# Kernel tuning notes

Hardware: AMD Instinct MI355X
Metric: run time of the kernel (lower is better)

## Reference

```python
import jax, jax.numpy as jnp
import numpy as np

B, T, C = 4, 4096, 512
DFF = 4 * C


def setup_inputs() -> dict:
    key = jax.random.key(0)
    ks = jax.random.split(key, 8)
    s = 1.0 / np.sqrt(C)
    sf = 1.0 / np.sqrt(DFF)
    return {
        "inputs": jax.random.normal(ks[0], (B, T, C), dtype=jnp.float32),
        "Wq": jax.random.uniform(ks[1], (C, C), jnp.float32, -s, s),
        "Wk": jax.random.uniform(ks[2], (C, C), jnp.float32, -s, s),
        "Wv": jax.random.uniform(ks[3], (C, C), jnp.float32, -s, s),
        "W1": jax.random.uniform(ks[4], (C, DFF), jnp.float32, -s, s),
        "b1": jax.random.uniform(ks[5], (DFF,), jnp.float32, -s, s),
        "W2": jax.random.uniform(ks[6], (DFF, C), jnp.float32, -sf, sf),
        "b2": jax.random.uniform(ks[7], (C,), jnp.float32, -sf, sf),
    }


def reference(inputs, Wq, Wk, Wv, W1, b1, W2, b2):
    # Single-head causal self-attention, NO 1/sqrt(d) scaling (faithful to source)
    q = inputs @ Wq  # [B,T,C]
    k = inputs @ Wk
    v = inputs @ Wv
    scores = jnp.einsum("btc,bsc->bts", q, k)  # [B,T,T]
    Tdim = inputs.shape[1]
    causal = jnp.tril(jnp.ones((Tdim, Tdim), dtype=bool))
    scores = jnp.where(causal, scores, -jnp.inf)
    attn = jax.nn.softmax(scores, axis=-1)
    new_v = jnp.einsum("bts,bsc->btc", attn, v)  # [B,T,C]
    h = jax.nn.relu(new_v @ W1 + b1)  # [B,T,4C]
    return h @ W2 + b2  # [B,T,C]
```

## Files before the change

kernel.cpp:

```cpp
#include <hip/hip_runtime.h>
#include <stdint.h>

typedef __attribute__((ext_vector_type(8))) short bf16x8;
typedef __attribute__((ext_vector_type(8))) _Float16 f16x8;
typedef __attribute__((ext_vector_type(4))) float f32x4;
typedef __attribute__((ext_vector_type(4))) unsigned short us4;
typedef unsigned short u16;

#define DEVI static __device__ __forceinline__

#define Bb 4
#define Tt 4096
#define Cch 512
#define DFFd 2048
#define Mrows (Bb*Tt)
#define TRI 8650752ull

DEVI u16 f2bf(float f){
  union{float f;unsigned u;} v; v.f = f;
  unsigned r = v.u + 0x7FFFu + ((v.u >> 16) & 1u);
  return (u16)(r >> 16);
}
DEVI u16 f2h(float f){
  union{_Float16 h; u16 u;} v; v.h = (_Float16)f; return v.u;
}
DEVI float h2f(u16 h){
  union{u16 u; _Float16 h;} v; v.u = h; return (float)v.h;
}
DEVI size_t PANE(int q){ return (size_t)8192 * (size_t)(q*(q+1)); }

DEVI void gload16(const void* g, void* l){
  __builtin_amdgcn_global_load_lds((const __attribute__((address_space(1))) unsigned int*)g,
                                   (__attribute__((address_space(3))) unsigned int*)l, 16, 0, 0);
}

#define RDSWZ(l15, l4) (((l4)*16) ^ ((((l15) >> 1) & 3) << 4))
#define SRCSWZ(lane) ((((lane) & 3)*8) ^ ((((lane) >> 3) & 3) << 3))

DEVI void stage256x64_w8(const u16* __restrict__ base, int ld, char* lds, int w, int lane){
  #pragma unroll
  for(int i = 0; i < 4; i++){
    int s = i & 1;
    int chunk = w + (i >> 1)*8;
    int row = chunk*16 + (lane >> 2);
    int col = s*32 + SRCSWZ(lane);
    gload16(base + (size_t)row * ld + col, lds + s*16384 + chunk*1024 + lane*16);
  }
}
DEVI void stage128x64_w8(const u16* __restrict__ base, int ld, char* lds, int w, int lane){
  #pragma unroll
  for(int i = 0; i < 2; i++){
    int s = i;
    int row = w*16 + (lane >> 2);
    int col = s*32 + SRCSWZ(lane);
    gload16(base + (size_t)row * ld + col, lds + s*8192 + w*1024 + lane*16);
  }
}

__global__ void k_cast_f16(const float* __restrict__ in, u16* __restrict__ out, int n){
  int i = (blockIdx.x * blockDim.x + threadIdx.x) * 4;
  if(i < n){
    float4 f = *(const float4*)(in + i);
    us4 o; o.x = f2h(f.x); o.y = f2h(f.y); o.z = f2h(f.z); o.w = f2h(f.w);
    *(us4*)(out + i) = o;
  }
}

__global__ void k_transpose_f32_f16(const float* __restrict__ in, u16* __restrict__ out,
                                    int inStride, int outStride){
  __shared__ float tile[32][33];
  int c0 = blockIdx.x * 32, r0 = blockIdx.y * 32;
  int tx = threadIdx.x, ty = threadIdx.y;
  #pragma unroll
  for(int j = 0; j < 4; j++)
    tile[ty + 8*j][tx] = in[(size_t)(r0 + ty + 8*j) * inStride + c0 + tx];
  __syncthreads();
  #pragma unroll
  for(int j = 0; j < 4; j++)
    out[(size_t)(c0 + ty + 8*j) * outStride + r0 + tx] = f2h(tile[tx][ty + 8*j]);
}

__global__ void k_transpose_f32_bf16(const float* __restrict__ in, u16* __restrict__ out,
                                     int inStride, int outStride){
  __shared__ float tile[32][33];
  int c0 = blockIdx.x * 32, r0 = blockIdx.y * 32;
  int tx = threadIdx.x, ty = threadIdx.y;
  #pragma unroll
  for(int j = 0; j < 4; j++)
    tile[ty + 8*j][tx] = in[(size_t)(r0 + ty + 8*j) * inStride + c0 + tx];
  __syncthreads();
  #pragma unroll
  for(int j = 0; j < 4; j++)
    out[(size_t)(c0 + ty + 8*j) * outStride + r0 + tx] = f2bf(tile[tx][ty + 8*j]);
}

DEVI void core_f16_256(const u16* __restrict__ A, const u16* __restrict__ B,
                       int lda, int ldb, int K, u16* As, u16* Bs, f32x4 (&acc)[4][4]){
  const int t = threadIdx.x;
  const int lane = t & 63, w = t >> 6;
  const int l15 = lane & 15, l4 = lane >> 4;
  const int wr = (w >> 1) * 64, wc = (w & 1) * 64;
  const int ro = RDSWZ(l15, l4);
  for(int kt = 0; kt < K; kt += 64){
    __syncthreads();
    stage256x64_w8(A + kt, lda, (char*)As, w, lane);
    stage128x64_w8(B + kt, ldb, (char*)Bs, w, lane);
    __syncthreads();
    f16x8 af[2][4], bfr[2][4];
    #pragma unroll
    for(int s = 0; s < 2; s++){
      #pragma unroll
      for(int mi = 0; mi < 4; mi++)
        af[s][mi] = *(const f16x8*)((const char*)As + s*16384 + (wr + mi*16 + l15)*64 + ro);
      #pragma unroll
      for(int ni = 0; ni < 4; ni++)
        bfr[s][ni] = *(const f16x8*)((const char*)Bs + s*8192 + (wc + ni*16 + l15)*64 + ro);
    }
    #pragma unroll
    for(int s = 0; s < 2; s++)
      #pragma unroll
      for(int mi = 0; mi < 4; mi++)
        #pragma unroll
        for(int ni = 0; ni < 4; ni++)
          acc[mi][ni] = __builtin_amdgcn_mfma_f32_16x16x32_f16(af[s][mi], bfr[s][ni], acc[mi][ni], 0, 0, 0);
  }
}

DEVI void core_bf16_256(const u16* __restrict__ A, const u16* __restrict__ B,
                        int lda, int ldb, int K, u16* As, u16* Bs, f32x4 (&acc)[4][4]){
  const int t = threadIdx.x;
  const int lane = t & 63, w = t >> 6;
  const int l15 = lane & 15, l4 = lane >> 4;
  const int wr = (w >> 1) * 64, wc = (w & 1) * 64;
  const int ro = RDSWZ(l15, l4);
  for(int kt = 0; kt < K; kt += 64){
    __syncthreads();
    stage256x64_w8(A + kt, lda, (char*)As, w, lane);
    stage128x64_w8(B + kt, ldb, (char*)Bs, w, lane);
    __syncthreads();
    bf16x8 af[2][4], bfr[2][4];
    #pragma unroll
    for(int s = 0; s < 2; s++){
      #pragma unroll
      for(int mi = 0; mi < 4; mi++)
        af[s][mi] = *(const bf16x8*)((const char*)As + s*16384 + (wr + mi*16 + l15)*64 + ro);
      #pragma unroll
      for(int ni = 0; ni < 4; ni++)
        bfr[s][ni] = *(const bf16x8*)((const char*)Bs + s*8192 + (wc + ni*16 + l15)*64 + ro);
    }
    #pragma unroll
    for(int s = 0; s < 2; s++)
      #pragma unroll
      for(int mi = 0; mi < 4; mi++)
        #pragma unroll
        for(int ni = 0; ni < 4; ni++)
          acc[mi][ni] = __builtin_amdgcn_mfma_f32_16x16x32_bf16(af[s][mi], bfr[s][ni], acc[mi][ni], 0, 0, 0);
  }
}

__global__ __launch_bounds__(512) void k_qkv(const u16* __restrict__ Xf,
                                             const u16* __restrict__ Wt,
                                             u16* __restrict__ QK,
                                             u16* __restrict__ Vg){
  __shared__ u16 As[16384], Bs[8192];
  const int bm = blockIdx.x * 256, bn = blockIdx.y * 128;
  f32x4 acc[4][4] = {};
  core_f16_256(Xf + (size_t)bm*512, Wt + (size_t)bn*512, 512, 512, 512, As, Bs, acc);
  const int t = threadIdx.x, lane = t & 63, w = t >> 6;
  const int l15 = lane & 15, l4 = lane >> 4;
  const int wr = (w >> 1) * 64, wc = (w & 1) * 64;
  #pragma unroll
  for(int mi = 0; mi < 4; mi++)
    #pragma unroll
    for(int ni = 0; ni < 4; ni++){
      int col = bn + wc + ni*16 + l15;
      #pragma unroll
      for(int r = 0; r < 4; r++){
        int row = bm + wr + mi*16 + l4*4 + r;
        u16 h = f2h(acc[mi][ni][r]);
        if(col < 1024){
          QK[(size_t)row * 1024 + col] = h;
        } else {
          int c = col - 1024;
          int b = row >> 12, tq = row & 4095;
          Vg[(size_t)b*Cch*Tt + ((size_t)(tq >> 5) * 512 + c) * 32 + (tq & 31)] = h;
        }
      }
    }
}

__global__ __launch_bounds__(512) void k_score(const u16* __restrict__ QK, int b0,
                                               u16* __restrict__ Sp){
  const int kt = blockIdx.x, qy = 15 - blockIdx.y;
  if(kt > 2*qy + 1) return;
  const int zb = blockIdx.z;
  const u16* QKb = QK + (size_t)(b0 + zb) * Tt * 1024;
  u16* Spz = Sp + (size_t)zb * TRI;
  __shared__ u16 As[16384], Bs[8192];
  const u16* A = QKb + (size_t)(qy*256) * 1024;
  const u16* B = QKb + (size_t)(kt*128) * 1024 + 512;
  f32x4 acc[4][4] = {};
  core_f16_256(A, B, 1024, 1024, 512, As, Bs, acc);
  const int t = threadIdx.x, lane = t & 63, w = t >> 6;
  const int l15 = lane & 15, l4 = lane >> 4;
  const int wr = (w >> 1) * 64, wc = (w & 1) * 64;
  const int qt_row = qy*2 + (wr >> 7);
  if(kt > qt_row) return;
  const int ldc = (qt_row + 1) * 128;
  const int rof = wr & 64;
  u16* C = Spz + PANE(qt_row) + (size_t)kt*128;
  const bool diag = (kt == qt_row);
  #pragma unroll
  for(int mi = 0; mi < 4; mi++)
    #pragma unroll
    for(int ni = 0; ni < 4; ni++){
      int cl = wc + ni*16 + l15;
      #pragma unroll
      for(int r = 0; r < 4; r++){
        int rl = rof + mi*16 + l4*4 + r;
        float v = acc[mi][ni][r];
        if(diag && cl > rl) v = -__builtin_inff();
        C[(size_t)rl * ldc + cl] = f2h(v);
      }
    }
}

__global__ __launch_bounds__(256) void k_softmax(u16* __restrict__ Sp){
  u16* Spz = Sp + (size_t)blockIdx.z * TRI;
  const int w = threadIdx.x >> 6, lane = threadIdx.x & 63;
  const int r = (1023 - blockIdx.x) * 4 + w;
  const int qt = r >> 7;
  const int nc = qt + 1;
  const int L = nc * 128;
  const size_t base = PANE(qt) + (size_t)(r & 127) * L;
  ushort2* rp = (ushort2*)(Spz + base);
  float2 v[32];
  float mx = -__builtin_inff();
  #pragma unroll
  for(int c = 0; c < 32; c++) if(c < nc){
    ushort2 h = rp[c*64 + lane];
    v[c].x = h2f(h.x); v[c].y = h2f(h.y);
    mx = fmaxf(mx, fmaxf(v[c].x, v[c].y));
  }
  #pragma unroll
  for(int s = 1; s < 64; s <<= 1) mx = fmaxf(mx, __shfl_xor(mx, s));
  float sm = 0.f;
  #pragma unroll
  for(int c = 0; c < 32; c++) if(c < nc){
    v[c].x = __expf(v[c].x - mx);
    v[c].y = __expf(v[c].y - mx);
    sm += v[c].x + v[c].y;
  }
  #pragma unroll
  for(int s = 1; s < 64; s <<= 1) sm += __shfl_xor(sm, s);
  const float inv = 1.f / sm;
  #pragma unroll
  for(int c = 0; c < 32; c++) if(c < nc){
    ushort2 o; o.x = f2h(v[c].x * inv); o.y = f2h(v[c].y * inv);
    rp[c*64 + lane] = o;
  }
}

__global__ __launch_bounds__(512) void k_pv(const u16* __restrict__ Pp, const u16* __restrict__ Vg,
                                            u16* __restrict__ NV, int b0){
  const int nc = blockIdx.x, qt = 31 - blockIdx.y, zb = blockIdx.z;
  const int L = (qt + 1) * 128;
  __shared__ u16 As[8192], Bs[8192];
  const u16* A = Pp + (size_t)zb * TRI + PANE(qt);
  const u16* Vgb = Vg + (size_t)(b0 + zb) * Cch * Tt;
  const int t = threadIdx.x, lane = t & 63, w = t >> 6;
  const int l15 = lane & 15, l4 = lane >> 4;
  const int wr = (w >> 1) * 32, wc = (w & 1) * 64;
  const int ro = RDSWZ(l15, l4);
  f32x4 acc[2][4] = {};
  for(int kt = 0; kt < L; kt += 64){
    __syncthreads();
    stage128x64_w8(A + kt, L, (char*)As, w, lane);
    const size_t kvb0 = (size_t)(kt >> 5) * 16384 + nc*4096;
    #pragma unroll
    for(int i = 0; i < 2; i++){
      int s = i;
      int crow = w*16 + (lane >> 2);
      int kvo = SRCSWZ(lane);
      gload16(Vgb + kvb0 + (size_t)s*16384 + (size_t)crow*32 + kvo,
              (char*)Bs + s*8192 + w*1024 + lane*16);
    }
    __syncthreads();
    f16x8 af[2][2], bfr[2][4];
    #pragma unroll
    for(int s = 0; s < 2; s++){
      #pragma unroll
      for(int mi = 0; mi < 2; mi++)
        af[s][mi] = *(const f16x8*)((const char*)As + s*8192 + (wr + mi*16 + l15)*64 + ro);
      #pragma unroll
      for(int ni = 0; ni < 4; ni++)
        bfr[s][ni] = *(const f16x8*)((const char*)Bs + s*8192 + (wc + ni*16 + l15)*64 + ro);
    }
    #pragma unroll
    for(int s = 0; s < 2; s++)
      #pragma unroll
      for(int mi = 0; mi < 2; mi++)
        #pragma unroll
        for(int ni = 0; ni < 4; ni++)
          acc[mi][ni] = __builtin_amdgcn_mfma_f32_16x16x32_f16(af[s][mi], bfr[s][ni], acc[mi][ni], 0, 0, 0);
  }
  u16* Cb = NV + ((size_t)(b0 + zb) * Tt + qt*128) * Cch + nc*128;
  #pragma unroll
  for(int mi = 0; mi < 2; mi++)
    #pragma unroll
    for(int ni = 0; ni < 4; ni++){
      int cl = wc + ni*16 + l15;
      #pragma unroll
      for(int r = 0; r < 4; r++){
        int rl = wr + mi*16 + l4*4 + r;
        Cb[(size_t)rl * Cch + cl] = f2bf(acc[mi][ni][r]);
      }
    }
}

__global__ __launch_bounds__(512) void k_ffn1(const u16* __restrict__ A,
                                              const u16* __restrict__ Bt,
                                              u16* __restrict__ Hout,
                                              const float* __restrict__ bias){
  __shared__ u16 As[16384], Bs[8192];
  const int bm = blockIdx.x * 256, bn = blockIdx.y * 128;
  f32x4 acc[4][4] = {};
  core_bf16_256(A + (size_t)bm*512, Bt + (size_t)bn*512, 512, 512, 512, As, Bs, acc);
  const int t = threadIdx.x, lane = t & 63, w = t >> 6;
  const int l15 = lane & 15, l4 = lane >> 4;
  const int wr = (w >> 1) * 64, wc = (w & 1) * 64;
  #pragma unroll
  for(int mi = 0; mi < 4; mi++)
    #pragma unroll
    for(int ni = 0; ni < 4; ni++){
      int col = bn + wc + ni*16 + l15;
      float bv = bias[col];
      #pragma unroll
      for(int r = 0; r < 4; r++){
        int row = bm + wr + mi*16 + l4*4 + r;
        float v = acc[mi][ni][r] + bv;
        v = v > 0.f ? v : 0.f;
        Hout[(size_t)row * DFFd + col] = f2bf(v);
      }
    }
}

__global__ __launch_bounds__(512) void k_ffn2(const u16* __restrict__ A,
                                              const u16* __restrict__ Bt,
                                              float* __restrict__ out,
                                              const float* __restrict__ bias){
  __shared__ u16 As[8192], Bs[8192];
  const int bn = blockIdx.x * 128, bm = blockIdx.y * 128;
  const int t = threadIdx.x, lane = t & 63, w = t >> 6;
  const int l15 = lane & 15, l4 = lane >> 4;
  const int wr = (w >> 1) * 32, wc = (w & 1) * 64;
  const int ro = RDSWZ(l15, l4);
  const u16* Ap = A + (size_t)bm*2048;
  const u16* Bp = Bt + (size_t)bn*2048;
  f32x4 acc[2][4] = {};
  for(int kt = 0; kt < 2048; kt += 64){
    __syncthreads();
    stage128x64_w8(Ap + kt, 2048, (char*)As, w, lane);
    stage128x64_w8(Bp + kt, 2048, (char*)Bs, w, lane);
    __syncthreads();
    bf16x8 af[2][2], bfr[2][4];
    #pragma unroll
    for(int s = 0; s < 2; s++){
      #pragma unroll
      for(int mi = 0; mi < 2; mi++)
        af[s][mi] = *(const bf16x8*)((const char*)As + s*8192 + (wr + mi*16 + l15)*64 + ro);
      #pragma unroll
      for(int ni = 0; ni < 4; ni++)
        bfr[s][ni] = *(const bf16x8*)((const char*)Bs + s*8192 + (wc + ni*16 + l15)*64 + ro);
    }
    #pragma unroll
    for(int s = 0; s < 2; s++)
      #pragma unroll
      for(int mi = 0; mi < 2; mi++)
        #pragma unroll
        for(int ni = 0; ni < 4; ni++)
          acc[mi][ni] = __builtin_amdgcn_mfma_f32_16x16x32_bf16(af[s][mi], bfr[s][ni], acc[mi][ni], 0, 0, 0);
  }
  #pragma unroll
  for(int mi = 0; mi < 2; mi++)
    #pragma unroll
    for(int ni = 0; ni < 4; ni++){
      int col = bn + wc + ni*16 + l15;
      float bv = bias[col];
      #pragma unroll
      for(int r = 0; r < 4; r++){
        int row = bm + wr + mi*16 + l4*4 + r;
        out[(size_t)row * Cch + col] = acc[mi][ni][r] + bv;
      }
    }
}

extern "C" void kernel_launch(void* const* d_in, const int* in_sizes, int n_in,
                              void* d_out, int out_size, void* d_ws, size_t ws_size,
                              hipStream_t stream){
  (void)in_sizes; (void)n_in; (void)out_size;
  const float* X  = (const float*)d_in[0];
  const float* Wq = (const float*)d_in[1];
  const float* Wk = (const float*)d_in[2];
  const float* Wv = (const float*)d_in[3];
  const float* W1 = (const float*)d_in[4];
  const float* b1 = (const float*)d_in[5];
  const float* W2 = (const float*)d_in[6];
  const float* b2 = (const float*)d_in[7];
  float* out = (float*)d_out;

  const size_t MB = 1024ull*1024ull;
  const size_t PANE_B = (size_t)TRI * 2;
  char* ws = (char*)d_ws;

  int nb = 1;
  if(ws_size >= 4*PANE_B + 71*MB) nb = 4;
  else if(ws_size >= 2*PANE_B + 71*MB) nb = 2;

  u16*   Sp = (u16*)ws;
  u16*   Xf = (u16*)ws;
  u16*   H  = (u16*)ws;
  size_t off = (size_t)nb * PANE_B;
  u16*   QK   = (u16*)(ws + off);  off += 32*MB;
  u16*   Vg   = (u16*)(ws + off);  off += 16*MB;
  u16*   NV   = (u16*)(ws + off);  off += 16*MB;
  u16*   Wt   = (u16*)(ws + off);  off += 2*MB;
  u16*   W1t  = (u16*)(ws + off);  off += 2*MB;
  u16*   W2t  = (u16*)(ws + off);

  dim3 tb(32, 8);

  k_cast_f16<<<Mrows*Cch/4/256, 256, 0, stream>>>(X, Xf, Mrows*Cch);

  k_transpose_f32_f16<<<dim3(16,16), tb, 0, stream>>>(Wq, Wt,            512, 512);
  k_transpose_f32_f16<<<dim3(16,16), tb, 0, stream>>>(Wk, Wt +  512*512, 512, 512);
  k_transpose_f32_f16<<<dim3(16,16), tb, 0, stream>>>(Wv, Wt + 1024*512, 512, 512);
  k_transpose_f32_bf16<<<dim3(64,16), tb, 0, stream>>>(W1, W1t, 2048, 512);
  k_transpose_f32_bf16<<<dim3(16,64), tb, 0, stream>>>(W2, W2t, 512, 2048);

  k_qkv<<<dim3(64, 12), 512, 0, stream>>>(Xf, Wt, QK, Vg);

  for(int b0 = 0; b0 < Bb; b0 += nb){
    k_score<<<dim3(32, 16, nb), 512, 0, stream>>>(QK, b0, Sp);
    k_softmax<<<dim3(1024, 1, nb), 256, 0, stream>>>(Sp);
    k_pv<<<dim3(4, 32, nb), 512, 0, stream>>>(Sp, Vg, NV, b0);
  }

  k_ffn1<<<dim3(64, 16), 512, 0, stream>>>(NV, W1t, H, b1);
  k_ffn2<<<dim3(4, 128), 512, 0, stream>>>(H, W2t, out, b2);
}
```

Measured before the change: 326.1 us.

## Enlarge score and FFN1 GEMM tiles to 256x256 with 16-wave blocks

Switches the attention score GEMM and the first FFN GEMM from 256x128 tiles with 8 waves to 256x256 tiles with 16 waves (1024 threads), adding a staging helper and new core loops. Each block now reuses its A tile across twice as many output columns, which cuts global and LDS traffic per FLOP. In the score kernel, causal masking and tile skipping are redone per 128-column subtile inside the wider block. The cost is fewer blocks, lower occupancy per CU and more wasted work on diagonal blocks, where the upper-triangle half is computed and thrown away.

```diff
diff --git a/kernel.cpp b/kernel.cpp
--- a/kernel.cpp
+++ b/kernel.cpp
@@ -56,6 +56,15 @@
     gload16(base + (size_t)row * ld + col, lds + s*8192 + w*1024 + lane*16);
   }
 }
+DEVI void stage256x64_w16(const u16* __restrict__ base, int ld, char* lds, int w, int lane){
+  #pragma unroll
+  for(int i = 0; i < 2; i++){
+    int s = i;
+    int row = w*16 + (lane >> 2);
+    int col = s*32 + SRCSWZ(lane);
+    gload16(base + (size_t)row * ld + col, lds + s*16384 + w*1024 + lane*16);
+  }
+}
 
 __global__ void k_cast_f16(const float* __restrict__ in, u16* __restrict__ out, int n){
   int i = (blockIdx.x * blockDim.x + threadIdx.x) * 4;
@@ -126,17 +135,49 @@
   }
 }
 
-DEVI void core_bf16_256(const u16* __restrict__ A, const u16* __restrict__ B,
-                        int lda, int ldb, int K, u16* As, u16* Bs, f32x4 (&acc)[4][4]){
+DEVI void core_f16_1k(const u16* __restrict__ A, const u16* __restrict__ B,
+                      int lda, int ldb, int K, u16* As, u16* Bs, f32x4 (&acc)[4][4]){
   const int t = threadIdx.x;
   const int lane = t & 63, w = t >> 6;
   const int l15 = lane & 15, l4 = lane >> 4;
-  const int wr = (w >> 1) * 64, wc = (w & 1) * 64;
+  const int wr = (w >> 2) * 64, wc = (w & 3) * 64;
   const int ro = RDSWZ(l15, l4);
   for(int kt = 0; kt < K; kt += 64){
     __syncthreads();
-    stage256x64_w8(A + kt, lda, (char*)As, w, lane);
-    stage128x64_w8(B + kt, ldb, (char*)Bs, w, lane);
+    stage256x64_w16(A + kt, lda, (char*)As, w, lane);
+    stage256x64_w16(B + kt, ldb, (char*)Bs, w, lane);
+    __syncthreads();
+    f16x8 af[2][4], bfr[2][4];
+    #pragma unroll
+    for(int s = 0; s < 2; s++){
+      #pragma unroll
+      for(int mi = 0; mi < 4; mi++)
+        af[s][mi] = *(const f16x8*)((const char*)As + s*16384 + (wr + mi*16 + l15)*64 + ro);
+      #pragma unroll
+      for(int ni = 0; ni < 4; ni++)
+        bfr[s][ni] = *(const f16x8*)((const char*)Bs + s*16384 + (wc + ni*16 + l15)*64 + ro);
+    }
+    #pragma unroll
+    for(int s = 0; s < 2; s++)
+      #pragma unroll
+      for(int mi = 0; mi < 4; mi++)
+        #pragma unroll
+        for(int ni = 0; ni < 4; ni++)
+          acc[mi][ni] = __builtin_amdgcn_mfma_f32_16x16x32_f16(af[s][mi], bfr[s][ni], acc[mi][ni], 0, 0, 0);
+  }
+}
+
+DEVI void core_bf16_1k(const u16* __restrict__ A, const u16* __restrict__ B,
+                       int lda, int ldb, int K, u16* As, u16* Bs, f32x4 (&acc)[4][4]){
+  const int t = threadIdx.x;
+  const int lane = t & 63, w = t >> 6;
+  const int l15 = lane & 15, l4 = lane >> 4;
+  const int wr = (w >> 2) * 64, wc = (w & 3) * 64;
+  const int ro = RDSWZ(l15, l4);
+  for(int kt = 0; kt < K; kt += 64){
+    __syncthreads();
+    stage256x64_w16(A + kt, lda, (char*)As, w, lane);
+    stage256x64_w16(B + kt, ldb, (char*)Bs, w, lane);
     __syncthreads();
     bf16x8 af[2][4], bfr[2][4];
     #pragma unroll
@@ -146,7 +187,7 @@
         af[s][mi] = *(const bf16x8*)((const char*)As + s*16384 + (wr + mi*16 + l15)*64 + ro);
       #pragma unroll
       for(int ni = 0; ni < 4; ni++)
-        bfr[s][ni] = *(const bf16x8*)((const char*)Bs + s*8192 + (wc + ni*16 + l15)*64 + ro);
+        bfr[s][ni] = *(const bf16x8*)((const char*)Bs + s*16384 + (wc + ni*16 + l15)*64 + ro);
     }
     #pragma unroll
     for(int s = 0; s < 2; s++)
@@ -189,38 +230,40 @@
     }
 }
 
-__global__ __launch_bounds__(512) void k_score(const u16* __restrict__ QK, int b0,
-                                               u16* __restrict__ Sp){
-  const int kt = blockIdx.x, qy = 15 - blockIdx.y;
-  if(kt > 2*qy + 1) return;
+__global__ __launch_bounds__(1024) void k_score(const u16* __restrict__ QK, int b0,
+                                                u16* __restrict__ Sp){
+  const int kp = blockIdx.x, qy = 15 - blockIdx.y;
+  if(kp > qy) return;
   const int zb = blockIdx.z;
   const u16* QKb = QK + (size_t)(b0 + zb) * Tt * 1024;
   u16* Spz = Sp + (size_t)zb * TRI;
-  __shared__ u16 As[16384], Bs[8192];
+  __shared__ u16 As[16384], Bs[16384];
   const u16* A = QKb + (size_t)(qy*256) * 1024;
-  const u16* B = QKb + (size_t)(kt*128) * 1024 + 512;
+  const u16* B = QKb + (size_t)(kp*256) * 1024 + 512;
   f32x4 acc[4][4] = {};
-  core_f16_256(A, B, 1024, 1024, 512, As, Bs, acc);
+  core_f16_1k(A, B, 1024, 1024, 512, As, Bs, acc);
   const int t = threadIdx.x, lane = t & 63, w = t >> 6;
   const int l15 = lane & 15, l4 = lane >> 4;
-  const int wr = (w >> 1) * 64, wc = (w & 1) * 64;
+  const int wr = (w >> 2) * 64, wc = (w & 3) * 64;
   const int qt_row = qy*2 + (wr >> 7);
-  if(kt > qt_row) return;
   const int ldc = (qt_row + 1) * 128;
   const int rof = wr & 64;
-  u16* C = Spz + PANE(qt_row) + (size_t)kt*128;
-  const bool diag = (kt == qt_row);
+  u16* C = Spz + PANE(qt_row);
   #pragma unroll
   for(int mi = 0; mi < 4; mi++)
     #pragma unroll
     for(int ni = 0; ni < 4; ni++){
-      int cl = wc + ni*16 + l15;
+      int csub = wc + ni*16;
+      int kt_tile = kp*2 + (csub >> 7);
+      if(kt_tile > qt_row) continue;
+      int colin = (csub & 127) + l15;
+      const bool diag = (kt_tile == qt_row);
       #pragma unroll
       for(int r = 0; r < 4; r++){
         int rl = rof + mi*16 + l4*4 + r;
         float v = acc[mi][ni][r];
-        if(diag && cl > rl) v = -__builtin_inff();
-        C[(size_t)rl * ldc + cl] = f2h(v);
+        if(diag && colin > rl) v = -__builtin_inff();
+        C[(size_t)rl * ldc + kt_tile*128 + colin] = f2h(v);
       }
     }
 }
@@ -318,17 +361,17 @@
     }
 }
 
-__global__ __launch_bounds__(512) void k_ffn1(const u16* __restrict__ A,
-                                              const u16* __restrict__ Bt,
-                                              u16* __restrict__ Hout,
-                                              const float* __restrict__ bias){
-  __shared__ u16 As[16384], Bs[8192];
-  const int bm = blockIdx.x * 256, bn = blockIdx.y * 128;
+__global__ __launch_bounds__(1024) void k_ffn1(const u16* __restrict__ A,
+                                               const u16* __restrict__ Bt,
+                                               u16* __restrict__ Hout,
+                                               const float* __restrict__ bias){
+  __shared__ u16 As[16384], Bs[16384];
+  const int bm = blockIdx.x * 256, bn = blockIdx.y * 256;
   f32x4 acc[4][4] = {};
-  core_bf16_256(A + (size_t)bm*512, Bt + (size_t)bn*512, 512, 512, 512, As, Bs, acc);
+  core_bf16_1k(A + (size_t)bm*512, Bt + (size_t)bn*512, 512, 512, 512, As, Bs, acc);
   const int t = threadIdx.x, lane = t & 63, w = t >> 6;
   const int l15 = lane & 15, l4 = lane >> 4;
-  const int wr = (w >> 1) * 64, wc = (w & 1) * 64;
+  const int wr = (w >> 2) * 64, wc = (w & 3) * 64;
   #pragma unroll
   for(int mi = 0; mi < 4; mi++)
     #pragma unroll
@@ -441,11 +484,11 @@
   k_qkv<<<dim3(64, 12), 512, 0, stream>>>(Xf, Wt, QK, Vg);
 
   for(int b0 = 0; b0 < Bb; b0 += nb){
-    k_score<<<dim3(32, 16, nb), 512, 0, stream>>>(QK, b0, Sp);
+    k_score<<<dim3(16, 16, nb), 1024, 0, stream>>>(QK, b0, Sp);
     k_softmax<<<dim3(1024, 1, nb), 256, 0, stream>>>(Sp);
     k_pv<<<dim3(4, 32, nb), 512, 0, stream>>>(Sp, Vg, NV, b0);
   }
 
-  k_ffn1<<<dim3(64, 16), 512, 0, stream>>>(NV, W1t, H, b1);
+  k_ffn1<<<dim3(64, 8), 1024, 0, stream>>>(NV, W1t, H, b1);
   k_ffn2<<<dim3(4, 128), 512, 0, stream>>>(H, W2t, out, b2);
 }
```

Result: slower. 348.3 us (+6.8%).

## Shrink score kernel tile to 128x128 to skip wasted upper-triangle work

Applied to the files above, without the earlier changes.

The causal score kernel now uses 128x128 output tiles per block instead of 256x128, with a custom K-loop that stages 128x64 panels and uses 16x16x32 f16 MFMA. Blocks above the diagonal exit early at the finer granularity, so half-masked 256-row tiles no longer compute rows that are discarded. The cost is less reuse of the K panel per block, twice as many blocks, and less MFMA work per wave to hide shared-memory loads.

```diff
diff --git a/kernel.cpp b/kernel.cpp
--- a/kernel.cpp
+++ b/kernel.cpp
@@ -191,33 +191,53 @@
 
 __global__ __launch_bounds__(512) void k_score(const u16* __restrict__ QK, int b0,
                                                u16* __restrict__ Sp){
-  const int kt = blockIdx.x, qy = 15 - blockIdx.y;
-  if(kt > 2*qy + 1) return;
+  const int kt = blockIdx.x, qt = 31 - blockIdx.y;
+  if(kt > qt) return;
   const int zb = blockIdx.z;
   const u16* QKb = QK + (size_t)(b0 + zb) * Tt * 1024;
   u16* Spz = Sp + (size_t)zb * TRI;
-  __shared__ u16 As[16384], Bs[8192];
-  const u16* A = QKb + (size_t)(qy*256) * 1024;
+  __shared__ u16 As[8192], Bs[8192];
+  const u16* A = QKb + (size_t)(qt*128) * 1024;
   const u16* B = QKb + (size_t)(kt*128) * 1024 + 512;
-  f32x4 acc[4][4] = {};
-  core_f16_256(A, B, 1024, 1024, 512, As, Bs, acc);
   const int t = threadIdx.x, lane = t & 63, w = t >> 6;
   const int l15 = lane & 15, l4 = lane >> 4;
-  const int wr = (w >> 1) * 64, wc = (w & 1) * 64;
-  const int qt_row = qy*2 + (wr >> 7);
-  if(kt > qt_row) return;
-  const int ldc = (qt_row + 1) * 128;
-  const int rof = wr & 64;
-  u16* C = Spz + PANE(qt_row) + (size_t)kt*128;
-  const bool diag = (kt == qt_row);
-  #pragma unroll
-  for(int mi = 0; mi < 4; mi++)
+  const int wr = (w >> 1) * 32, wc = (w & 1) * 64;
+  const int ro = RDSWZ(l15, l4);
+  f32x4 acc[2][4] = {};
+  for(int kk = 0; kk < 512; kk += 64){
+    __syncthreads();
+    stage128x64_w8(A + kk, 1024, (char*)As, w, lane);
+    stage128x64_w8(B + kk, 1024, (char*)Bs, w, lane);
+    __syncthreads();
+    f16x8 af[2][2], bfr[2][4];
+    #pragma unroll
+    for(int s = 0; s < 2; s++){
+      #pragma unroll
+      for(int mi = 0; mi < 2; mi++)
+        af[s][mi] = *(const f16x8*)((const char*)As + s*8192 + (wr + mi*16 + l15)*64 + ro);
+      #pragma unroll
+      for(int ni = 0; ni < 4; ni++)
+        bfr[s][ni] = *(const f16x8*)((const char*)Bs + s*8192 + (wc + ni*16 + l15)*64 + ro);
+    }
+    #pragma unroll
+    for(int s = 0; s < 2; s++)
+      #pragma unroll
+      for(int mi = 0; mi < 2; mi++)
+        #pragma unroll
+        for(int ni = 0; ni < 4; ni++)
+          acc[mi][ni] = __builtin_amdgcn_mfma_f32_16x16x32_f16(af[s][mi], bfr[s][ni], acc[mi][ni], 0, 0, 0);
+  }
+  const int ldc = (qt + 1) * 128;
+  u16* C = Spz + PANE(qt) + (size_t)kt*128;
+  const bool diag = (kt == qt);
+  #pragma unroll
+  for(int mi = 0; mi < 2; mi++)
     #pragma unroll
     for(int ni = 0; ni < 4; ni++){
       int cl = wc + ni*16 + l15;
       #pragma unroll
       for(int r = 0; r < 4; r++){
-        int rl = rof + mi*16 + l4*4 + r;
+        int rl = wr + mi*16 + l4*4 + r;
         float v = acc[mi][ni][r];
         if(diag && cl > rl) v = -__builtin_inff();
         C[(size_t)rl * ldc + cl] = f2h(v);
@@ -441,7 +461,7 @@
   k_qkv<<<dim3(64, 12), 512, 0, stream>>>(Xf, Wt, QK, Vg);
 
   for(int b0 = 0; b0 < Bb; b0 += nb){
-    k_score<<<dim3(32, 16, nb), 512, 0, stream>>>(QK, b0, Sp);
+    k_score<<<dim3(32, 32, nb), 512, 0, stream>>>(QK, b0, Sp);
     k_softmax<<<dim3(1024, 1, nb), 256, 0, stream>>>(Sp);
     k_pv<<<dim3(4, 32, nb), 512, 0, stream>>>(Sp, Vg, NV, b0);
   }
```

Result: no change. 324.5 us, median of 2 (-0.5%).
